# Kernel optimization log

Measured on AMD Instinct MI355X. Metric: run time of the kernel, lower is better.

Reference implementation:

```python
import jax, jax.numpy as jnp
import numpy as np
import math

NUM_HEADS = 4


def setup_inputs() -> dict:
    key = jax.random.key(0)
    ks = jax.random.split(key, 6)
    N, L, C = 8, 8192, 256
    x = jax.random.normal(ks[0], (N, L, C), dtype=jnp.float32)
    attention_mask = jax.random.randint(ks[1], (N, 1, L, 1), 0, 2).astype(jnp.int32)
    qkv_w = jax.random.normal(ks[2], (3 * C, C), dtype=jnp.float32) * (1.0 / np.sqrt(C))
    proj_w = jax.random.normal(ks[3], (C, C), dtype=jnp.float32) * (1.0 / np.sqrt(C))
    proj_b = jax.random.normal(ks[4], (C,), dtype=jnp.float32) * 0.01
    dconv_w = jax.random.normal(ks[5], (NUM_HEADS, 1, 9, 1), dtype=jnp.float32) * 0.1
    return {"x": x, "attention_mask": attention_mask, "qkv_w": qkv_w,
            "proj_w": proj_w, "proj_b": proj_b, "dconv_w": dconv_w}


def _l2norm(t):
    return t / jnp.linalg.norm(t, axis=-1, keepdims=True)


def reference(x, attention_mask, qkv_w, proj_w, proj_b, dconv_w):
    N, L, C = x.shape
    H = NUM_HEADS
    D = C // H
    # qkv projection: (N, L, 3C) -> (3, N, H, L, D)
    qkv = (x @ qkv_w.T).reshape(N, L, 3, H, D).transpose(2, 0, 3, 1, 4)
    q, k, v = qkv[0], qkv[1], qkv[2]
    # masked_fill on q before normalization (faithful to original)
    q = jnp.where(attention_mask == 0, jnp.float32(-1e9), q)
    q = _l2norm(q)
    k = _l2norm(k)
    # depthwise conv over L axis of v: (N, H, L, D), kernel (9,1), groups=H
    dconv_v = jax.lax.conv_general_dilated(
        v, dconv_w, window_strides=(1, 1), padding=((4, 4), (0, 0)),
        dimension_numbers=("NCHW", "OIHW", "NCHW"), feature_group_count=H)
    # linear attention: (k^T v) is (N, H, D, D)
    kv = jnp.einsum("nhld,nhle->nhde", k, v)
    out = 0.5 * v + (1.0 / math.pi) * jnp.einsum("nhld,nhde->nhle", q, kv)
    out = _l2norm(out)
    out = out + dconv_v
    out = out.transpose(0, 2, 1, 3).reshape(N, L, C)
    return out @ proj_w.T + proj_b
```

## Files before the change

kernel.cpp:

```cpp
#include <hip/hip_runtime.h>
#include <hip/hip_bf16.h>
#include <math.h>

#define N_ 8
#define L_ 8192
#define C_ 256
#define H_ 4
#define D_ 64
#define NH_ (N_*H_)
#define NCH 32
#define CHUNK (L_/NCH)
#define Q_ ((size_t)N_*H_*L_*D_)

typedef float f32x4 __attribute__((ext_vector_type(4)));
typedef short short8 __attribute__((ext_vector_type(8)));

__device__ inline ushort f2b(float f){
  uint x = __float_as_uint(f);
  uint r = (x + 0x7fffu + ((x >> 16) & 1u)) >> 16;
  return (ushort)r;
}
__device__ inline ushort f2b_hw(float f){
  __hip_bfloat16 h = __float2bfloat16(f);
  return *reinterpret_cast<ushort*>(&h);
}
__device__ inline float b2f(ushort u){
  return __uint_as_float(((uint)u) << 16);
}
__device__ inline uint pk2h(float a, float b){
  return (uint)f2b_hw(a) | ((uint)f2b_hw(b) << 16);
}
__device__ inline void unpack8(uint4 p, float* f){
  f[0]=__uint_as_float(p.x<<16); f[1]=__uint_as_float(p.x&0xffff0000u);
  f[2]=__uint_as_float(p.y<<16); f[3]=__uint_as_float(p.y&0xffff0000u);
  f[4]=__uint_as_float(p.z<<16); f[5]=__uint_as_float(p.z&0xffff0000u);
  f[6]=__uint_as_float(p.w<<16); f[7]=__uint_as_float(p.w&0xffff0000u);
}

#define GLD16(g, l) __builtin_amdgcn_global_load_lds( \
    (const __attribute__((address_space(1))) void*)(g), \
    (__attribute__((address_space(3))) void*)(l), 16, 0, 0)

__global__ __launch_bounds__(256) void conv_w(const float* __restrict__ w,
                                              ushort* __restrict__ wb) {
  const int i = (blockIdx.x*256 + threadIdx.x) * 4;
  float4 f = *(const float4*)(w + i);
  *(ushort4*)&wb[i] = make_ushort4(f2b(f.x), f2b(f.y), f2b(f.z), f2b(f.w));
}

__global__ __launch_bounds__(512) void qkv_gemm_mfma2(const float* __restrict__ x,
                                                      const ushort* __restrict__ wb,
                                                      const int* __restrict__ mask,
                                                      ushort* __restrict__ qb,
                                                      ushort* __restrict__ kb,
                                                      ushort* __restrict__ vb) {
  __shared__ ushort As[128][64];
  __shared__ ushort Bs[256][64];
  const int tid  = threadIdx.x;
  const int lane = tid & 63;
  const int wid  = tid >> 6, wm = wid >> 2, wn = wid & 3;
  const int r15  = lane & 15, kg = lane >> 4;
  const int lrow8 = lane >> 3;
  const int lgrp  = lane & 7;
  const int bid = blockIdx.x;
  const int wg  = (bid & 7)*192 + (bid >> 3);
  const int bx  = wg / 3, by = wg % 3;
  const int gm0 = bx * 128;
  const int gn0 = by * 256;

  const int arow = tid >> 2;
  const int ag0  = (tid & 3) << 1;
  const float* asrc = x + (size_t)(gm0 + arow)*C_ + (ag0 << 3);

  f32x4 acc[4][4] = {};

  for (int k0 = 0; k0 < C_; k0 += 64) {
    float4 f0 = *(const float4*)(asrc + k0);
    float4 f1 = *(const float4*)(asrc + k0 + 4);
    float4 f2 = *(const float4*)(asrc + k0 + 8);
    float4 f3 = *(const float4*)(asrc + k0 + 12);
    if (k0) __syncthreads();
#pragma unroll
    for (int r = 0; r < 4; ++r) {
      const int row = wid*32 + r*8 + lrow8;
      const int gc  = k0 + ((lgrp ^ (row & 7)) << 3);
      GLD16(wb + (size_t)(gn0 + row)*C_ + gc, &Bs[wid*32 + r*8][0]);
    }
    {
      uint4 p0 = make_uint4(pk2h(f0.x,f0.y), pk2h(f0.z,f0.w),
                            pk2h(f1.x,f1.y), pk2h(f1.z,f1.w));
      uint4 p1 = make_uint4(pk2h(f2.x,f2.y), pk2h(f2.z,f2.w),
                            pk2h(f3.x,f3.y), pk2h(f3.z,f3.w));
      *(uint4*)&As[arow][( ag0      ^ (arow & 7)) << 3] = p0;
      *(uint4*)&As[arow][((ag0 + 1) ^ (arow & 7)) << 3] = p1;
    }
    __syncthreads();
#pragma unroll
    for (int ks = 0; ks < 2; ++ks) {
      short8 a[4], b[4];
#pragma unroll
      for (int mi = 0; mi < 4; ++mi) {
        const int row = wm*64 + mi*16 + r15;
        a[mi] = *(const short8*)&As[row][((ks*4 + kg) ^ (row & 7)) << 3];
      }
#pragma unroll
      for (int ni = 0; ni < 4; ++ni) {
        const int row = wn*64 + ni*16 + r15;
        b[ni] = *(const short8*)&Bs[row][((ks*4 + kg) ^ (row & 7)) << 3];
      }
#pragma unroll
      for (int mi = 0; mi < 4; ++mi)
#pragma unroll
        for (int ni = 0; ni < 4; ++ni)
          acc[mi][ni] = __builtin_amdgcn_mfma_f32_16x16x32_bf16(
              a[mi], b[ni], acc[mi][ni], 0, 0, 0);
    }
  }

  const int sh = by*4 + wn;
  const int s = sh >> 2, h = sh & 3;
  ushort* dst = (s == 0) ? qb : (s == 1) ? kb : vb;
#pragma unroll
  for (int mi = 0; mi < 4; ++mi) {
    const int rbase = gm0 + wm*64 + mi*16 + (kg << 2);
#pragma unroll
    for (int j = 0; j < 4; ++j) {
      const int gr = rbase + j;
      const int nn = gr >> 13, l = gr & (L_-1);
      float v0 = acc[mi][0][j], v1 = acc[mi][1][j],
            v2 = acc[mi][2][j], v3 = acc[mi][3][j];
      if (s < 2) {
        float ss = v0*v0 + v1*v1 + v2*v2 + v3*v3;
        ss += __shfl_xor(ss, 1); ss += __shfl_xor(ss, 2);
        ss += __shfl_xor(ss, 4); ss += __shfl_xor(ss, 8);
        const float inv = 1.0f / sqrtf(ss);
        v0 *= inv; v1 *= inv; v2 *= inv; v3 *= inv;
      }
      const bool masked = (s == 0) && (mask[(size_t)nn*L_ + l] == 0);
      const size_t base = (((size_t)nn*H_ + h)*L_ + l)*D_ + r15;
      if (masked) {
        const ushort mb = 0xBE00u;
        dst[base] = mb; dst[base+16] = mb; dst[base+32] = mb; dst[base+48] = mb;
      } else {
        dst[base]    = f2b(v0); dst[base+16] = f2b(v1);
        dst[base+32] = f2b(v2); dst[base+48] = f2b(v3);
      }
    }
  }
}

__global__ __launch_bounds__(256, 8) void kv_partial(const ushort* __restrict__ kb,
                                                     const ushort* __restrict__ vb,
                                                     ushort* __restrict__ part) {
  const int nh = blockIdx.x, ch = blockIdx.y;
  const size_t base = ((size_t)nh*L_ + (size_t)ch*CHUNK) * 64;
  __shared__ float ks[32][68];
  __shared__ float vs[32][68];
  const int tid = threadIdx.x;
  const int dB = tid >> 4, eB = tid & 15;
  const int lr = tid >> 3, lc = (tid & 7) << 3;
  float acc[4][4] = {};
  for (int l0 = 0; l0 < CHUNK; l0 += 32) {
    uint4 kp = *(const uint4*)(kb + base + (size_t)(l0+lr)*64 + lc);
    uint4 vp = *(const uint4*)(vb + base + (size_t)(l0+lr)*64 + lc);
    float kf[8], vf[8];
    unpack8(kp, kf); unpack8(vp, vf);
    *(float4*)&ks[lr][lc]   = make_float4(kf[0],kf[1],kf[2],kf[3]);
    *(float4*)&ks[lr][lc+4] = make_float4(kf[4],kf[5],kf[6],kf[7]);
    *(float4*)&vs[lr][lc]   = make_float4(vf[0],vf[1],vf[2],vf[3]);
    *(float4*)&vs[lr][lc+4] = make_float4(vf[4],vf[5],vf[6],vf[7]);
    __syncthreads();
#pragma unroll 8
    for (int l = 0; l < 32; ++l) {
      float4 k4 = *(const float4*)&ks[l][dB*4];
      float4 v4 = *(const float4*)&vs[l][eB*4];
      float kk[4] = {k4.x,k4.y,k4.z,k4.w};
      float vv[4] = {v4.x,v4.y,v4.z,v4.w};
#pragma unroll
      for (int i = 0; i < 4; ++i)
#pragma unroll
        for (int j = 0; j < 4; ++j)
          acc[i][j] += kk[i]*vv[j];
    }
    __syncthreads();
  }
  ushort* P = part + ((size_t)nh*NCH + ch)*4096;
#pragma unroll
  for (int i = 0; i < 4; ++i)
#pragma unroll
    for (int j = 0; j < 4; ++j)
      P[(dB*4+i)*64 + eB*4+j] = f2b(acc[i][j]);
}

__global__ __launch_bounds__(256) void kv_reduce(const ushort* __restrict__ part,
                                                 ushort* __restrict__ kvbT) {
  const int nh = blockIdx.x;
  const int i0 = blockIdx.y*1024 + threadIdx.x*4;
  float s0 = 0.f, s1 = 0.f, s2 = 0.f, s3 = 0.f;
#pragma unroll
  for (int c = 0; c < NCH; ++c) {
    ushort4 p = *(const ushort4*)(part + ((size_t)nh*NCH + c)*4096 + i0);
    s0 += b2f(p.x); s1 += b2f(p.y); s2 += b2f(p.z); s3 += b2f(p.w);
  }
  const float ip = 0.31830988618379067f;
  const float r[4] = {s0*ip, s1*ip, s2*ip, s3*ip};
#pragma unroll
  for (int j = 0; j < 4; ++j) {
    const int i = i0 + j;
    const int d = i >> 6, e = i & 63;
    kvbT[(size_t)nh*4096 + e*64 + d] = f2b(r[j]);
  }
}

__global__ __launch_bounds__(256, 4) void attn_proj3(const ushort* __restrict__ qb,
                                                     const ushort* __restrict__ vb,
                                                     const ushort* __restrict__ kvbT,
                                                     const float* __restrict__ dwc,
                                                     const ushort* __restrict__ pwb,
                                                     const float* __restrict__ pb,
                                                     float* __restrict__ out) {
  __shared__ ushort vsm[4][40][72];
  __shared__ ushort attn_s[32][260];
  const int tid = threadIdx.x;
  const int lane = tid & 63;
  const int w = tid >> 6;
  const int r15 = lane & 15, kg = lane >> 4;
  const int n = blockIdx.y;
  const int l0 = blockIdx.x * 32;

  for (int f = tid; f < 1280; f += 256) {
    const int h = f / 320, rem = f % 320;
    const int row = rem >> 3, c0 = (rem & 7) << 3;
    const int lg = l0 - 4 + row;
    uint4 val = make_uint4(0,0,0,0);
    if ((unsigned)lg < (unsigned)L_)
      val = *(const uint4*)(vb + (((size_t)(n*4+h)*L_ + lg) << 6) + c0);
    *(uint4*)&vsm[h][row][c0] = val;
  }

  const int nh = n*4 + w;
  f32x4 acc[2][4] = {};
  {
    const ushort* qbase = qb + ((size_t)nh*L_ + l0)*64;
    const ushort* kvb = kvbT + (size_t)nh*4096;
#pragma unroll
    for (int ks = 0; ks < 2; ++ks) {
      const int kofs = ks*32 + kg*8;
      short8 a[2], b[4];
#pragma unroll
      for (int mi = 0; mi < 2; ++mi)
        a[mi] = *(const short8*)(qbase + (size_t)(mi*16 + r15)*64 + kofs);
#pragma unroll
      for (int ni = 0; ni < 4; ++ni)
        b[ni] = *(const short8*)(kvb + (ni*16 + r15)*64 + kofs);
#pragma unroll
      for (int mi = 0; mi < 2; ++mi)
#pragma unroll
        for (int ni = 0; ni < 4; ++ni)
          acc[mi][ni] = __builtin_amdgcn_mfma_f32_16x16x32_bf16(
              a[mi], b[ni], acc[mi][ni], 0, 0, 0);
    }
  }
  __syncthreads();

  {
    float wcv[9];
#pragma unroll
    for (int j = 0; j < 9; ++j) wcv[j] = dwc[w*9 + j];
    float win[9];
#pragma unroll
    for (int j = 0; j < 9; ++j) win[j] = b2f(vsm[w][j][lane]);
#pragma unroll
    for (int r = 0; r < 32; ++r) {
      float cv = 0.f;
#pragma unroll
      for (int j = 0; j < 9; ++j) cv += win[j] * wcv[j];
      attn_s[r][w*64 + lane] = f2b(cv);
      if (r < 31) {
#pragma unroll
        for (int j = 0; j < 8; ++j) win[j] = win[j+1];
        win[8] = b2f(vsm[w][r + 9][lane]);
      }
    }
  }
  __syncthreads();

#pragma unroll
  for (int mi = 0; mi < 2; ++mi) {
#pragma unroll
    for (int j = 0; j < 4; ++j) {
      const int r = mi*16 + kg*4 + j;
      float t[4];
#pragma unroll
      for (int ni = 0; ni < 4; ++ni) {
        const int e = ni*16 + r15;
        t[ni] = acc[mi][ni][j] + 0.5f * b2f(vsm[w][r+4][e]);
      }
      float ss = t[0]*t[0] + t[1]*t[1] + t[2]*t[2] + t[3]*t[3];
      ss += __shfl_xor(ss, 1); ss += __shfl_xor(ss, 2);
      ss += __shfl_xor(ss, 4); ss += __shfl_xor(ss, 8);
      const float inv = 1.0f / sqrtf(ss);
#pragma unroll
      for (int ni = 0; ni < 4; ++ni) {
        const int e = ni*16 + r15;
        const float cv = b2f(attn_s[r][w*64 + e]);
        attn_s[r][w*64 + e] = f2b(t[ni]*inv + cv);
      }
    }
  }
  __syncthreads();

  f32x4 acc2[2][4] = {};
  const ushort* pwq = pwb + (size_t)(w*64)*256;
#pragma unroll
  for (int ks = 0; ks < 8; ++ks) {
    const int kofs = ks*32 + kg*8;
    short8 a[2], b[4];
#pragma unroll
    for (int mi = 0; mi < 2; ++mi)
      a[mi] = *(const short8*)&attn_s[mi*16 + r15][kofs];
#pragma unroll
    for (int ni = 0; ni < 4; ++ni)
      b[ni] = *(const short8*)(pwq + (size_t)(ni*16 + r15)*256 + kofs);
#pragma unroll
    for (int mi = 0; mi < 2; ++mi)
#pragma unroll
      for (int ni = 0; ni < 4; ++ni)
        acc2[mi][ni] = __builtin_amdgcn_mfma_f32_16x16x32_bf16(
            a[mi], b[ni], acc2[mi][ni], 0, 0, 0);
  }
#pragma unroll
  for (int ni = 0; ni < 4; ++ni) {
    const int o = w*64 + ni*16 + r15;
    const float bias = pb[o];
#pragma unroll
    for (int mi = 0; mi < 2; ++mi) {
#pragma unroll
      for (int j = 0; j < 4; ++j) {
        const int l = l0 + mi*16 + kg*4 + j;
        out[((size_t)n*L_ + l)*C_ + o] = acc2[mi][ni][j] + bias;
      }
    }
  }
}

extern "C" void kernel_launch(void* const* d_in, const int* in_sizes, int n_in,
                              void* d_out, int out_size, void* d_ws, size_t ws_size,
                              hipStream_t stream) {
  const float* x      = (const float*)d_in[0];
  const int*   mask   = (const int*)d_in[1];
  const float* qkv_w  = (const float*)d_in[2];
  const float* proj_w = (const float*)d_in[3];
  const float* proj_b = (const float*)d_in[4];
  const float* dconv_w= (const float*)d_in[5];
  float* out = (float*)d_out;

  ushort* qb = (ushort*)d_ws;
  ushort* kb = qb + Q_;
  ushort* vb = kb + Q_;
  ushort* part = vb + Q_;
  ushort* kvbT = part + (size_t)NH_*NCH*4096;
  ushort* wb   = kvbT + (size_t)NH_*4096;
  ushort* pwb  = wb + 768*256;

  conv_w        <<<dim3(192),       256, 0, stream>>>(qkv_w, wb);
  conv_w        <<<dim3(64),        256, 0, stream>>>(proj_w, pwb);
  qkv_gemm_mfma2<<<dim3(1536),      512, 0, stream>>>(x, wb, mask, qb, kb, vb);
  kv_partial    <<<dim3(NH_, NCH),  256, 0, stream>>>(kb, vb, part);
  kv_reduce     <<<dim3(NH_, 4),    256, 0, stream>>>(part, kvbT);
  attn_proj3    <<<dim3(L_/32, N_), 256, 0, stream>>>(qb, vb, kvbT, dconv_w,
                                                      pwb, proj_b, out);
}
```

Measured before the change: 155.4 us.

## Restructure QKV GEMM: full-K A tile in LDS, B fragments read directly from global

Measured after the change: 176.0 us. 13.2% more time.

```diff
diff --git a/kernel.cpp b/kernel.cpp
--- a/kernel.cpp
+++ b/kernel.cpp
@@ -37,10 +37,6 @@
   f[6]=__uint_as_float(p.w<<16); f[7]=__uint_as_float(p.w&0xffff0000u);
 }
 
-#define GLD16(g, l) __builtin_amdgcn_global_load_lds( \
-    (const __attribute__((address_space(1))) void*)(g), \
-    (__attribute__((address_space(3))) void*)(l), 16, 0, 0)
-
 __global__ __launch_bounds__(256) void conv_w(const float* __restrict__ w,
                                               ushort* __restrict__ wb) {
   const int i = (blockIdx.x*256 + threadIdx.x) * 4;
@@ -48,73 +44,65 @@
   *(ushort4*)&wb[i] = make_ushort4(f2b(f.x), f2b(f.y), f2b(f.z), f2b(f.w));
 }
 
-__global__ __launch_bounds__(512) void qkv_gemm_mfma2(const float* __restrict__ x,
-                                                      const ushort* __restrict__ wb,
-                                                      const int* __restrict__ mask,
-                                                      ushort* __restrict__ qb,
-                                                      ushort* __restrict__ kb,
-                                                      ushort* __restrict__ vb) {
-  __shared__ ushort As[128][64];
-  __shared__ ushort Bs[256][64];
+__global__ __launch_bounds__(256, 4) void qkv_gemm_mfma3(const float* __restrict__ x,
+                                                         const ushort* __restrict__ wb,
+                                                         const int* __restrict__ mask,
+                                                         ushort* __restrict__ qb,
+                                                         ushort* __restrict__ kb,
+                                                         ushort* __restrict__ vb) {
+  __shared__ ushort As[64][256];
   const int tid  = threadIdx.x;
   const int lane = tid & 63;
-  const int wid  = tid >> 6, wm = wid >> 2, wn = wid & 3;
+  const int wn   = tid >> 6;
   const int r15  = lane & 15, kg = lane >> 4;
-  const int lrow8 = lane >> 3;
-  const int lgrp  = lane & 7;
   const int bid = blockIdx.x;
-  const int wg  = (bid & 7)*192 + (bid >> 3);
+  const int wg  = (bid & 7)*384 + (bid >> 3);
   const int bx  = wg / 3, by = wg % 3;
-  const int gm0 = bx * 128;
+  const int gm0 = bx * 64;
   const int gn0 = by * 256;
 
-  const int arow = tid >> 2;
-  const int ag0  = (tid & 3) << 1;
-  const float* asrc = x + (size_t)(gm0 + arow)*C_ + (ag0 << 3);
-
-  f32x4 acc[4][4] = {};
-
-  for (int k0 = 0; k0 < C_; k0 += 64) {
-    float4 f0 = *(const float4*)(asrc + k0);
-    float4 f1 = *(const float4*)(asrc + k0 + 4);
-    float4 f2 = *(const float4*)(asrc + k0 + 8);
-    float4 f3 = *(const float4*)(asrc + k0 + 12);
-    if (k0) __syncthreads();
+  {
+    const int arow = tid >> 2;
+    const int acg  = tid & 3;
+    const float* asrc = x + (size_t)(gm0 + arow)*C_ + acg*16;
 #pragma unroll
     for (int r = 0; r < 4; ++r) {
-      const int row = wid*32 + r*8 + lrow8;
-      const int gc  = k0 + ((lgrp ^ (row & 7)) << 3);
-      GLD16(wb + (size_t)(gn0 + row)*C_ + gc, &Bs[wid*32 + r*8][0]);
-    }
-    {
+      const float* p = asrc + r*64;
+      float4 f0 = *(const float4*)(p);
+      float4 f1 = *(const float4*)(p + 4);
+      float4 f2 = *(const float4*)(p + 8);
+      float4 f3 = *(const float4*)(p + 12);
       uint4 p0 = make_uint4(pk2h(f0.x,f0.y), pk2h(f0.z,f0.w),
                             pk2h(f1.x,f1.y), pk2h(f1.z,f1.w));
       uint4 p1 = make_uint4(pk2h(f2.x,f2.y), pk2h(f2.z,f2.w),
                             pk2h(f3.x,f3.y), pk2h(f3.z,f3.w));
-      *(uint4*)&As[arow][( ag0      ^ (arow & 7)) << 3] = p0;
-      *(uint4*)&As[arow][((ag0 + 1) ^ (arow & 7)) << 3] = p1;
-    }
-    __syncthreads();
-#pragma unroll
-    for (int ks = 0; ks < 2; ++ks) {
-      short8 a[4], b[4];
-#pragma unroll
-      for (int mi = 0; mi < 4; ++mi) {
-        const int row = wm*64 + mi*16 + r15;
-        a[mi] = *(const short8*)&As[row][((ks*4 + kg) ^ (row & 7)) << 3];
-      }
-#pragma unroll
-      for (int ni = 0; ni < 4; ++ni) {
-        const int row = wn*64 + ni*16 + r15;
-        b[ni] = *(const short8*)&Bs[row][((ks*4 + kg) ^ (row & 7)) << 3];
-      }
-#pragma unroll
-      for (int mi = 0; mi < 4; ++mi)
-#pragma unroll
-        for (int ni = 0; ni < 4; ++ni)
-          acc[mi][ni] = __builtin_amdgcn_mfma_f32_16x16x32_bf16(
-              a[mi], b[ni], acc[mi][ni], 0, 0, 0);
-    }
+      const int ag = acg*2 + r*8;
+      *(uint4*)&As[arow][((ag    ) ^ (arow & 7)) << 3] = p0;
+      *(uint4*)&As[arow][((ag + 1) ^ (arow & 7)) << 3] = p1;
+    }
+  }
+  __syncthreads();
+
+  f32x4 acc[4][4] = {};
+  const ushort* bbase = wb + (size_t)(gn0 + wn*64)*C_;
+#pragma unroll 2
+  for (int ks = 0; ks < 8; ++ks) {
+    const int kofs = ks*32 + kg*8;
+    short8 a[4], b[4];
+#pragma unroll
+    for (int mi = 0; mi < 4; ++mi) {
+      const int row = mi*16 + r15;
+      a[mi] = *(const short8*)&As[row][((ks*4 + kg) ^ (row & 7)) << 3];
+    }
+#pragma unroll
+    for (int ni = 0; ni < 4; ++ni)
+      b[ni] = *(const short8*)(bbase + (size_t)(ni*16 + r15)*C_ + kofs);
+#pragma unroll
+    for (int mi = 0; mi < 4; ++mi)
+#pragma unroll
+      for (int ni = 0; ni < 4; ++ni)
+        acc[mi][ni] = __builtin_amdgcn_mfma_f32_16x16x32_bf16(
+            a[mi], b[ni], acc[mi][ni], 0, 0, 0);
   }
 
   const int sh = by*4 + wn;
@@ -122,7 +110,7 @@
   ushort* dst = (s == 0) ? qb : (s == 1) ? kb : vb;
 #pragma unroll
   for (int mi = 0; mi < 4; ++mi) {
-    const int rbase = gm0 + wm*64 + mi*16 + (kg << 2);
+    const int rbase = gm0 + mi*16 + (kg << 2);
 #pragma unroll
     for (int j = 0; j < 4; ++j) {
       const int gr = rbase + j;
@@ -365,7 +353,7 @@
 
   conv_w        <<<dim3(192),       256, 0, stream>>>(qkv_w, wb);
   conv_w        <<<dim3(64),        256, 0, stream>>>(proj_w, pwb);
-  qkv_gemm_mfma2<<<dim3(1536),      512, 0, stream>>>(x, wb, mask, qb, kb, vb);
+  qkv_gemm_mfma3<<<dim3(3072),      256, 0, stream>>>(x, wb, mask, qb, kb, vb);
   kv_partial    <<<dim3(NH_, NCH),  256, 0, stream>>>(kb, vb, part);
   kv_reduce     <<<dim3(NH_, 4),    256, 0, stream>>>(part, kvbT);
   attn_proj3    <<<dim3(L_/32, N_), 256, 0, stream>>>(qb, vb, kvbT, dconv_w,
```
